# Kernel optimization log

Hardware: AMD Instinct MI355X
Metric: run time of the kernel (lower is better)

Reference implementation:

```python
import jax, jax.numpy as jnp
import numpy as np

T, B, D, H = 512, 64, 512, 512


def setup_inputs() -> dict:
    key = jax.random.key(0)
    ks = jax.random.split(key, 3)
    inputs = jax.random.normal(ks[0], (T, B, D), dtype=jnp.float32)
    # Four gate linears (forget, input, update, output), each (D+H)->H.
    # Stack into a single [D+H, 4H] weight; columns ordered [f, i, g, o].
    bound = 1.0 / np.sqrt(D + H)  # torch.nn.Linear default init scale
    W = jax.random.uniform(ks[1], (D + H, 4 * H), dtype=jnp.float32, minval=-bound, maxval=bound)
    b = jax.random.uniform(ks[2], (4 * H,), dtype=jnp.float32, minval=-bound, maxval=bound)
    return {"inputs": inputs, "W": W, "b": b}


def _lstm_forward(inputs, W, b):
    Bsz = inputs.shape[1]
    Hd = W.shape[1] // 4
    h0 = jnp.zeros((Bsz, Hd), dtype=inputs.dtype)
    c0 = jnp.zeros((Bsz, Hd), dtype=inputs.dtype)

    def step(carry, x):
        hx, cx = carry
        combined = jnp.concatenate([x, hx], axis=1)  # [B, D+H]
        gates = combined @ W + b                      # [B, 4H]
        f, i, g, o = jnp.split(gates, 4, axis=1)
        f = jax.nn.sigmoid(f)
        i = jax.nn.sigmoid(i)
        g = jnp.tanh(g)
        o = jax.nn.sigmoid(o)
        cx = f * cx + i * g
        hx = o * jnp.tanh(cx)
        return (hx, cx), hx

    (hx, cx), outputs = jax.lax.scan(step, (h0, c0), inputs)
    return outputs, (hx, cx)


def reference(inputs, W, b):
    return _lstm_forward(inputs, W, b)
```

## Files before the change

kernel.cpp:

```cpp
#include <hip/hip_runtime.h>
#include <hip/hip_bf16.h>
#include <hip/hip_cooperative_groups.h>

namespace cg = cooperative_groups;

#define T_STEPS 512
#define RING_OFF 33554432u
#define FLAG_OFF 33685504u
#define WS_NEED  33689600u

typedef __attribute__((ext_vector_type(4))) float f32x4;
typedef __attribute__((ext_vector_type(8))) short short8;
typedef __attribute__((ext_vector_type(4))) unsigned int u32x4;

__device__ __forceinline__ short f2bf(float f) {
  __hip_bfloat16 h = __float2bfloat16(f);
  return *reinterpret_cast<short*>(&h);
}
__device__ __forceinline__ unsigned bfbits(float f) {
  __hip_bfloat16 h = __float2bfloat16(f);
  return (unsigned)*reinterpret_cast<unsigned short*>(&h);
}
__device__ __forceinline__ short8 as_s8(u32x4 v) {
  union { u32x4 u; short8 s; } x; x.u = v; return x.s;
}

__global__ __launch_bounds__(512, 2) void lstm_kernel(
    const float* __restrict__ X, const float* __restrict__ W,
    const float* __restrict__ Bv, float* __restrict__ Out,
    char* __restrict__ ws)
{
  __shared__ char BxL[32768];

  const int tid  = threadIdx.x;
  const int wg   = blockIdx.x;
  const int lane = tid & 63;
  const int wv   = tid >> 6;
  const int m    = wv >> 1;
  const int n    = wv & 1;
  const int c16  = lane & 15;
  const int kgrp = lane >> 4;
  const int gg   = c16 >> 2;
  const int q    = c16 & 3;

  char*     Xf    = ws;
  char*     ring  = ws + RING_OFF;
  unsigned* flags = (unsigned*)(ws + FLAG_OFF);

  if (tid == 0)
    __hip_atomic_store(&flags[wg * 16], 0u, __ATOMIC_RELAXED, __HIP_MEMORY_SCOPE_AGENT);

  for (int id = wg * 512 + tid; id < 512 * 64 * 64; id += 64 * 512) {
    const int c8  = id & 63;
    const int row = (id >> 6) & 63;
    const int t   = id >> 12;
    const float* xp = X + ((size_t)(t * 64 + row)) * 512 + c8 * 8;
    const float4 a = *(const float4*)xp;
    const float4 b = *(const float4*)(xp + 4);
    short8 v;
    v[0]=f2bf(a.x); v[1]=f2bf(a.y); v[2]=f2bf(a.z); v[3]=f2bf(a.w);
    v[4]=f2bf(b.x); v[5]=f2bf(b.y); v[6]=f2bf(b.z); v[7]=f2bf(b.w);
    *(short8*)(Xf + (size_t)t * 65536 + (row >> 4) * 16384 + (c8 >> 2) * 1024
               + ((((c8 & 3) << 4) | (row & 15))) * 16) = v;
  }
  __threadfence();
  cg::this_grid().sync();
  __builtin_amdgcn_fence(__ATOMIC_ACQUIRE, "agent");

  const int gcol = gg * 512 + wg * 8 + n * 4 + q;
  short8 Bh[16];
  #pragma unroll
  for (int kk = 0; kk < 16; ++kk) {
    short8 v;
    #pragma unroll
    for (int j = 0; j < 8; ++j)
      v[j] = f2bf(W[(size_t)(512 + kk * 32 + kgrp * 8 + j) * 2048 + gcol]);
    Bh[kk] = v;
  }
  if (wv < 2) {
    for (int f = 0; f < 16; ++f) {
      short8 v;
      #pragma unroll
      for (int j = 0; j < 8; ++j)
        v[j] = f2bf(W[(size_t)(f * 32 + kgrp * 8 + j) * 2048 + gcol]);
      *(short8*)(BxL + wv * 16384 + f * 1024 + lane * 16) = v;
    }
  }
  __syncthreads();
  const float bias = Bv[gcol];

  float cst[4] = {0.f, 0.f, 0.f, 0.f};

  u32x4 x0,x1,x2,x3,x4,x5,x6,x7,x8,x9,x10,x11,x12,x13,x14,x15;
  #define PFX4(base, o0, o1, o2, o3) \
    asm volatile( \
      "global_load_dwordx4 %0, %4, off\n\t"             \
      "global_load_dwordx4 %1, %4, off offset:1024\n\t" \
      "global_load_dwordx4 %2, %4, off offset:2048\n\t" \
      "global_load_dwordx4 %3, %4, off offset:3072"     \
      : "=&v"(o0), "=&v"(o1), "=&v"(o2), "=&v"(o3) : "v"(base))
  #define PFX(tt) do { \
    const char* xb_ = Xf + (size_t)(tt) * 65536 + m * 16384 + lane * 16; \
    PFX4(xb_,          x0,  x1,  x2,  x3);  \
    PFX4(xb_ + 4096,   x4,  x5,  x6,  x7);  \
    PFX4(xb_ + 8192,   x8,  x9,  x10, x11); \
    PFX4(xb_ + 12288,  x12, x13, x14, x15); \
  } while (0)

  PFX(0);

  for (int t = 0; t < T_STEPS; ++t) {
    asm volatile("s_waitcnt vmcnt(0)" ::: "memory");
    __builtin_amdgcn_sched_barrier(0);

    f32x4 ac0 = {0,0,0,0}, ac1 = {0,0,0,0}, ac2 = {0,0,0,0}, ac3 = {0,0,0,0};
    const char* bxp = BxL + n * 16384 + lane * 16;
    #define XM(i, ACC) ACC = __builtin_amdgcn_mfma_f32_16x16x32_bf16( \
        as_s8(x##i), *(const short8*)(bxp + i * 1024), ACC, 0, 0, 0)
    XM(0,ac0);  XM(1,ac1);  XM(2,ac2);  XM(3,ac3);
    XM(4,ac0);  XM(5,ac1);  XM(6,ac2);  XM(7,ac3);
    XM(8,ac0);  XM(9,ac1);  XM(10,ac2); XM(11,ac3);
    XM(12,ac0); XM(13,ac1); XM(14,ac2); XM(15,ac3);
    #undef XM

    if (t > 0) {
      if (wv == 0) {
        while (__hip_atomic_load(&flags[lane * 16], __ATOMIC_RELAXED,
                                 __HIP_MEMORY_SCOPE_AGENT) < (unsigned)t) {}
      }
      __builtin_amdgcn_s_barrier();
      __builtin_amdgcn_sched_barrier(0);

      const char* hp0 = ring + (size_t)((t - 1) & 1) * 65536 + m * 16384 + lane * 16;
      const char* hp1 = hp0 + 4096;
      const char* hp2 = hp0 + 8192;
      const char* hp3 = hp0 + 12288;
      u32x4 h0,h1,h2,h3,h4,h5,h6,h7,h8,h9,h10,h11,h12,h13,h14,h15;
      #define LDR(base, off, vv) \
        asm volatile("global_load_dwordx4 %0, %1, off offset:" off " sc0 sc1" \
                     : "=&v"(vv) : "v"(base))
      LDR(hp0, "0", h0);  LDR(hp0, "1024", h1);  LDR(hp0, "2048", h2);  LDR(hp0, "3072", h3);
      LDR(hp1, "0", h4);  LDR(hp1, "1024", h5);  LDR(hp1, "2048", h6);  LDR(hp1, "3072", h7);
      LDR(hp2, "0", h8);  LDR(hp2, "1024", h9);  LDR(hp2, "2048", h10); LDR(hp2, "3072", h11);
      LDR(hp3, "0", h12); LDR(hp3, "1024", h13); LDR(hp3, "2048", h14); LDR(hp3, "3072", h15);
      #undef LDR
      PFX(t == T_STEPS - 1 ? t : t + 1);

      asm volatile("s_waitcnt vmcnt(16)" ::: "memory");
      __builtin_amdgcn_sched_barrier(0);
      #define HM(i, ACC) ACC = __builtin_amdgcn_mfma_f32_16x16x32_bf16( \
          as_s8(h##i), Bh[i], ACC, 0, 0, 0)
      HM(0,ac0);  HM(1,ac1);  HM(2,ac2);  HM(3,ac3);
      HM(4,ac0);  HM(5,ac1);  HM(6,ac2);  HM(7,ac3);
      HM(8,ac0);  HM(9,ac1);  HM(10,ac2); HM(11,ac3);
      HM(12,ac0); HM(13,ac1); HM(14,ac2); HM(15,ac3);
      #undef HM
    } else {
      PFX(1);
    }

    float hv[4], cnv[4];
    #pragma unroll
    for (int r = 0; r < 4; ++r) {
      const float pre = ac0[r] + ac1[r] + ac2[r] + ac3[r] + bias;
      const float e   = __expf((gg == 2) ? -2.f * pre : -pre);
      const float act = (gg == 2) ? (2.f / (1.f + e) - 1.f) : (1.f / (1.f + e));
      const float vi  = __shfl_xor(act, 4);
      const float vg  = __shfl_xor(act, 8);
      const float cn  = act * cst[r] + vi * vg;
      if (gg == 0) cst[r] = cn;
      const float e2  = __expf(-2.f * cn);
      float tn = 2.f / (1.f + e2) - 1.f;
      tn = __shfl_xor(tn, 12);
      hv[r]  = act * tn;
      cnv[r] = cn;
    }

    {
      char* rp = ring + (size_t)(t & 1) * 65536 + m * 16384 + (wg >> 2) * 1024
               + (((wg & 3) << 4) + kgrp * 4) * 16 + (n * 4 + q) * 2;
      #pragma unroll
      for (int r = 0; r < 4; ++r) {
        const unsigned hb = bfbits(hv[r]);
        const unsigned pb = (unsigned)__shfl_xor((int)hb, 1);
        if (gg == 3 && !(q & 1))
          __hip_atomic_store((unsigned*)(rp + r * 16),
                             (hb & 0xffffu) | (pb << 16),
                             __ATOMIC_RELAXED, __HIP_MEMORY_SCOPE_AGENT);
      }
    }

    asm volatile("s_waitcnt vmcnt(0)" ::: "memory");
    __builtin_amdgcn_sched_barrier(0);
    __builtin_amdgcn_s_barrier();
    if (tid == 0) {
      unsigned tv = (unsigned)(t + 1);
      unsigned* fp = &flags[wg * 16];
      asm volatile("global_store_dword %0, %1, off sc0 sc1"
                   :: "v"(fp), "v"(tv) : "memory");
    }

    const int hc = wg * 8 + n * 4 + q;
    if (gg == 3) {
      float* op = Out + ((size_t)t * 64 + m * 16 + kgrp * 4) * 512 + hc;
      #pragma unroll
      for (int r = 0; r < 4; ++r) op[(size_t)r * 512] = hv[r];
      if (t == T_STEPS - 1) {
        #pragma unroll
        for (int r = 0; r < 4; ++r)
          Out[16777216u + (size_t)(m * 16 + kgrp * 4 + r) * 512 + hc] = hv[r];
      }
    }
    if (gg == 0 && t == T_STEPS - 1) {
      #pragma unroll
      for (int r = 0; r < 4; ++r)
        Out[16777216u + 32768u + (size_t)(m * 16 + kgrp * 4 + r) * 512 + hc] = cnv[r];
    }
  }
  #undef PFX
  #undef PFX4
}

extern "C" void kernel_launch(void* const* d_in, const int* in_sizes, int n_in,
                              void* d_out, int out_size, void* d_ws, size_t ws_size,
                              hipStream_t stream) {
  if (ws_size < (size_t)WS_NEED) return;

  const float* X  = (const float*)d_in[0];
  const float* W  = (const float*)d_in[1];
  const float* Bv = (const float*)d_in[2];
  float* Out = (float*)d_out;
  char*  ws  = (char*)d_ws;

  void* args[5];
  args[0] = (void*)&X;
  args[1] = (void*)&W;
  args[2] = (void*)&Bv;
  args[3] = (void*)&Out;
  args[4] = (void*)&ws;
  hipLaunchCooperativeKernel((const void*)lstm_kernel, dim3(64), dim3(512),
                             args, 0, stream);
}
```

Baseline: 2.382 ms.

## Pipeline flag polling, duplicate hidden-state ring per half, relax waits

Replaces the relaxed atomic spin on peer flags with a pipelined two-load polling loop using cache-bypassing loads and a wave-wide vote. It also writes each hidden-state chunk twice into a doubled ring so the two n-halves read from separate copies, pads the flags to a wider stride, lets the top-of-step wait keep 8 loads in flight, and lowers launch_bounds occupancy to 1. The intent is to cut inter-block sync latency and contention on the recurrent critical path, at the cost of extra stores and workspace.

```diff
diff --git a/kernel.cpp b/kernel.cpp
--- a/kernel.cpp
+++ b/kernel.cpp
@@ -6,8 +6,8 @@
 
 #define T_STEPS 512
 #define RING_OFF 33554432u
-#define FLAG_OFF 33685504u
-#define WS_NEED  33689600u
+#define FLAG_OFF 33816576u
+#define WS_NEED  33824768u
 
 typedef __attribute__((ext_vector_type(4))) float f32x4;
 typedef __attribute__((ext_vector_type(8))) short short8;
@@ -25,7 +25,7 @@
   union { u32x4 u; short8 s; } x; x.u = v; return x.s;
 }
 
-__global__ __launch_bounds__(512, 2) void lstm_kernel(
+__global__ __launch_bounds__(512, 1) void lstm_kernel(
     const float* __restrict__ X, const float* __restrict__ W,
     const float* __restrict__ Bv, float* __restrict__ Out,
     char* __restrict__ ws)
@@ -48,7 +48,7 @@
   unsigned* flags = (unsigned*)(ws + FLAG_OFF);
 
   if (tid == 0)
-    __hip_atomic_store(&flags[wg * 16], 0u, __ATOMIC_RELAXED, __HIP_MEMORY_SCOPE_AGENT);
+    __hip_atomic_store(&flags[wg * 32], 0u, __ATOMIC_RELAXED, __HIP_MEMORY_SCOPE_AGENT);
 
   for (int id = wg * 512 + tid; id < 512 * 64 * 64; id += 64 * 512) {
     const int c8  = id & 63;
@@ -110,7 +110,7 @@
   PFX(0);
 
   for (int t = 0; t < T_STEPS; ++t) {
-    asm volatile("s_waitcnt vmcnt(0)" ::: "memory");
+    asm volatile("s_waitcnt vmcnt(8)" ::: "memory");
     __builtin_amdgcn_sched_barrier(0);
 
     f32x4 ac0 = {0,0,0,0}, ac1 = {0,0,0,0}, ac2 = {0,0,0,0}, ac3 = {0,0,0,0};
@@ -124,14 +124,32 @@
     #undef XM
 
     if (t > 0) {
+      const unsigned tg = (unsigned)t;
       if (wv == 0) {
-        while (__hip_atomic_load(&flags[lane * 16], __ATOMIC_RELAXED,
-                                 __HIP_MEMORY_SCOPE_AGENT) < (unsigned)t) {}
+        const unsigned* fp = &flags[lane * 32];
+        unsigned va, vb;
+        asm volatile("global_load_dword %0, %1, off sc0 sc1"
+                     : "=&v"(va) : "v"(fp) : "memory");
+        for (;;) {
+          asm volatile("global_load_dword %0, %1, off sc0 sc1"
+                       : "=&v"(vb) : "v"(fp) : "memory");
+          asm volatile("s_waitcnt vmcnt(1)" ::: "memory");
+          __builtin_amdgcn_sched_barrier(0);
+          if (__all((int)(va >= tg))) break;
+          asm volatile("global_load_dword %0, %1, off sc0 sc1"
+                       : "=&v"(va) : "v"(fp) : "memory");
+          asm volatile("s_waitcnt vmcnt(1)" ::: "memory");
+          __builtin_amdgcn_sched_barrier(0);
+          if (__all((int)(vb >= tg))) break;
+        }
+        asm volatile("s_waitcnt vmcnt(0)" ::: "memory");
+        __builtin_amdgcn_sched_barrier(0);
       }
       __builtin_amdgcn_s_barrier();
       __builtin_amdgcn_sched_barrier(0);
 
-      const char* hp0 = ring + (size_t)((t - 1) & 1) * 65536 + m * 16384 + lane * 16;
+      const char* hp0 = ring + (size_t)((t - 1) & 1) * 131072 + (size_t)n * 65536
+                      + m * 16384 + lane * 16;
       const char* hp1 = hp0 + 4096;
       const char* hp2 = hp0 + 8192;
       const char* hp3 = hp0 + 12288;
@@ -177,16 +195,19 @@
     }
 
     {
-      char* rp = ring + (size_t)(t & 1) * 65536 + m * 16384 + (wg >> 2) * 1024
+      char* rp = ring + (size_t)(t & 1) * 131072 + m * 16384 + (wg >> 2) * 1024
                + (((wg & 3) << 4) + kgrp * 4) * 16 + (n * 4 + q) * 2;
       #pragma unroll
       for (int r = 0; r < 4; ++r) {
         const unsigned hb = bfbits(hv[r]);
         const unsigned pb = (unsigned)__shfl_xor((int)hb, 1);
-        if (gg == 3 && !(q & 1))
-          __hip_atomic_store((unsigned*)(rp + r * 16),
-                             (hb & 0xffffu) | (pb << 16),
-                             __ATOMIC_RELAXED, __HIP_MEMORY_SCOPE_AGENT);
+        if (gg == 3 && !(q & 1)) {
+          const unsigned pk = (hb & 0xffffu) | (pb << 16);
+          unsigned* p0 = (unsigned*)(rp + (size_t)r * 16);
+          asm volatile("global_store_dword %0, %2, off sc0 sc1\n\t"
+                       "global_store_dword %1, %2, off sc0 sc1"
+                       :: "v"(p0), "v"((char*)p0 + 65536), "v"(pk) : "memory");
+        }
       }
     }
 
@@ -195,7 +216,7 @@
     __builtin_amdgcn_s_barrier();
     if (tid == 0) {
       unsigned tv = (unsigned)(t + 1);
-      unsigned* fp = &flags[wg * 16];
+      unsigned* fp = &flags[wg * 32];
       asm volatile("global_store_dword %0, %1, off sc0 sc1"
                    :: "v"(fp), "v"(tv) : "memory");
     }
```

Measured after the change: 2.541 ms. +6.7%, slower.
